# Kernel tuning notes

Hardware: AMD Instinct MI355X
Metric: run time of the kernel (lower is better)

The kernel has to match this reference:

```python
import jax, jax.numpy as jnp
import numpy as np

N = 20000      # nodes
E = 320000     # edges
IN = 128       # in_channels
HID = 64       # hidden_channels (per-head out dim, concat=False -> mean over heads)
HEADS = 4
NEG_SLOPE = 0.2


def setup_inputs() -> dict:
    key = jax.random.key(0)
    ks = jax.random.split(key, 18)
    g = lambda i, shape: jax.random.normal(ks[i], shape, dtype=jnp.float32) * 0.05
    return {
        "x": jax.random.normal(ks[0], (N, IN), dtype=jnp.float32),
        "edge_index": jax.random.randint(ks[1], (2, E), 0, N),
        # GATConv params: lin weight (no bias in PyG lin), att_src/att_dst, out bias
        "W0": g(2, (IN, HEADS * HID)),
        "W1": g(3, (HID, HEADS * HID)),
        "W2": g(4, (HID, HEADS * HID)),
        "W3": g(5, (HID, HEADS * HID)),
        "a_src": g(6, (4, HEADS, HID)),
        "a_dst": g(7, (4, HEADS, HID)),
        "gat_b": g(8, (4, HID)),
        # residual projection for layer 0 (in_channels != hidden_channels)
        "res_W": g(9, (IN, HID)),
        "res_b": g(10, (HID,)),
        # edge classifier MLP: 2*HID -> HID -> HID -> 1
        "lin_W0": g(11, (2 * HID, HID)),
        "lin_b0": g(12, (HID,)),
        "lin_W1": g(13, (HID, HID)),
        "lin_b1": g(14, (HID,)),
        "lin_W2": g(15, (HID, 1)),
        "lin_b2": g(16, (1,)),
    }


def gat_conv(x, src, dst, W, asrc, adst, b, n):
    # x: [n, F_in]; src/dst: [E_tot] (self-loops included); W: [F_in, H*C]
    h = (x @ W).reshape(n, HEADS, HID)                     # [n, H, C]
    s_src = (h * asrc).sum(-1)                             # [n, H]
    s_dst = (h * adst).sum(-1)                             # [n, H]
    e = jax.nn.leaky_relu(s_src[src] + s_dst[dst], NEG_SLOPE)  # [E_tot, H]
    # segment softmax over incoming edges of each dst node
    m = jax.ops.segment_max(e, dst, num_segments=n)        # [n, H]
    p = jnp.exp(e - m[dst])
    z = jax.ops.segment_sum(p, dst, num_segments=n)
    alpha = p / z[dst]                                     # [E_tot, H]
    out = jax.ops.segment_sum(alpha[:, :, None] * h[src], dst, num_segments=n)  # [n, H, C]
    return out.mean(axis=1) + b                            # concat=False -> mean over heads


def reference(x, edge_index, W0, W1, W2, W3, a_src, a_dst, gat_b,
              res_W, res_b, lin_W0, lin_b0, lin_W1, lin_b1, lin_W2, lin_b2):
    n = x.shape[0]
    loop = jnp.arange(n)
    src = jnp.concatenate([edge_index[0], loop])  # PyG GATConv adds self-loops
    dst = jnp.concatenate([edge_index[1], loop])
    Ws = [W0, W1, W2, W3]
    h = x
    for i in range(4):
        h_prev = h
        h = gat_conv(h, src, dst, Ws[i], a_src[i], a_dst[i], gat_b[i], n)
        if i == 0:
            h = h + h_prev @ res_W + res_b   # projected residual
        else:
            h = h + h_prev
        h = jax.nn.elu(h)
    row, col = edge_index[0], edge_index[1]
    er = jnp.concatenate([h[row], h[col]], axis=1)        # [E, 2*HID]
    er = jax.nn.relu(er @ lin_W0 + lin_b0)                # shapes differ -> no residual
    er = jax.nn.relu(er @ lin_W1 + lin_b1 + er)           # shapes match -> residual
    logits = er @ lin_W2 + lin_b2                          # [E, 1]
    return logits
```

## Files before the change

### kernel.cpp

```cpp
#include <hip/hip_runtime.h>
#include <hip/hip_bf16.h>

#define NSLOPE 0.2f
#define MAXDEG 64

typedef short bf16x8 __attribute__((ext_vector_type(8)));
typedef float f32x4 __attribute__((ext_vector_type(4)));

__device__ __forceinline__ unsigned short f2b(float f) {
    unsigned u = __float_as_uint(f);
    unsigned r = (u + 0x7FFFu + ((u >> 16) & 1u)) >> 16;
    return (unsigned short)r;
}
__device__ __forceinline__ float b2f_lo(unsigned w) {
    return __uint_as_float(w << 16);
}
__device__ __forceinline__ float b2f_hi(unsigned w) {
    return __uint_as_float(w & 0xFFFF0000u);
}
__device__ __forceinline__ float b2f_s(short s) {
    return __uint_as_float(((unsigned)(unsigned short)s) << 16);
}
__device__ __forceinline__ unsigned packb(float lo, float hi) {
    return ((unsigned)f2b(hi) << 16) | (unsigned)f2b(lo);
}

__global__ __launch_bounds__(256) void prep_all(
    const float* __restrict__ W0, const float* __restrict__ W1,
    const float* __restrict__ W2, const float* __restrict__ W3,
    const float* __restrict__ resW, const float* __restrict__ linW0,
    const float* __restrict__ linW1, const float* __restrict__ linB0,
    const float* __restrict__ a_src, const float* __restrict__ a_dst,
    const float* __restrict__ gat_b, const float* __restrict__ res_b,
    short* __restrict__ WtC0e, short* __restrict__ WtC1,
    short* __restrict__ WtC2, short* __restrict__ WtC3,
    short* __restrict__ WtUV, short* __restrict__ WbT,
    float* __restrict__ wsd0, float* __restrict__ wsdL,
    float* __restrict__ bias128, float* __restrict__ gb0res,
    int* __restrict__ deg, int n) {
    const int bx = blockIdx.x;
    const int tid = threadIdx.x;
    if (bx == 0) {
        for (int idx = blockIdx.y * 256 + tid; idx < 64 * 640; idx += 256 * 16) {
            int j = idx / 640, k = idx - j * 640;
            float v;
            if (k < 512) {
                int h = k >> 7, kk = k & 127;
                v = W0[kk * 256 + h * 64 + j];
            } else {
                v = resW[(k - 512) * 64 + j];
            }
            WtC0e[idx] = (short)f2b(v);
        }
    } else if (bx <= 3) {
        const float* src = (bx == 1) ? W1 : (bx == 2) ? W2 : W3;
        short* dst = (bx == 1) ? WtC1 : (bx == 2) ? WtC2 : WtC3;
        for (int idx = blockIdx.y * 256 + tid; idx < 64 * 256; idx += 256 * 16) {
            int j = idx >> 8, rem = idx & 255;
            int h = rem >> 6, kk = rem & 63;
            dst[idx] = (short)f2b(src[kk * 256 + h * 64 + j]);
        }
    } else if (bx == 4) {
        if (blockIdx.y) return;
        for (int idx = tid; idx < 64 * 64; idx += 256) {
            int nn = idx >> 6, k = idx & 63;
            WtUV[idx] = (short)f2b(linW0[k * 64 + nn]);
        }
    } else if (bx == 5) {
        if (blockIdx.y) return;
        for (int idx = tid; idx < 64 * 64; idx += 256) {
            int nn = idx >> 6, k = idx & 63;
            WtUV[64 * 64 + idx] = (short)f2b(linW0[(k + 64) * 64 + nn]);
        }
    } else if (bx == 6) {
        if (blockIdx.y) return;
        for (int idx = tid; idx < 64 * 64; idx += 256) {
            int nn = idx >> 6, k = idx & 63;
            WbT[idx] = (short)f2b(linW1[k * 64 + nn]);
        }
    } else if (bx == 7) {
        if (blockIdx.y) return;
        if (tid < 128)
            bias128[tid] = (tid < 64) ? linB0[tid] : 0.f;
        else if (tid < 192)
            gb0res[tid - 128] = gat_b[tid - 128] + res_b[tid - 128];
    } else if (bx <= 11) {
        if (blockIdx.y) return;
        int l = bx - 8;
        const float* W = (l == 0) ? W0 : (l == 1) ? W1 : (l == 2) ? W2 : W3;
        const int K = (l == 0) ? 128 : 64;
        float* dst = (l == 0) ? wsd0 : wsdL + (l - 1) * 64 * 8;
        for (int idx = tid; idx < K * 8; idx += 256) {
            int k = idx >> 3, j = idx & 7, h = j & 3;
            const float* av = ((j < 4) ? a_src : a_dst) + l * 256 + h * 64;
            const float* wr = W + k * 256 + h * 64;
            float s = 0.f;
#pragma unroll 8
            for (int c = 0; c < 64; ++c) s += wr[c] * av[c];
            dst[k * 8 + j] = s;
        }
    } else {
        for (int i = blockIdx.y * 256 + tid; i < n; i += 256 * 16) deg[i] = 0;
    }
}

__global__ __launch_bounds__(256) void fill_convert(
    const int* __restrict__ ei, int* __restrict__ deg,
    unsigned short* __restrict__ csrS, int E, const float* __restrict__ x,
    const float* __restrict__ wsd0, unsigned* __restrict__ xb2,
    float* __restrict__ Ssrc, float* __restrict__ Sdst, int n, int eBlocks) {
    if ((int)blockIdx.x < eBlocks) {
        int e = blockIdx.x * 256 + threadIdx.x;
        if (e >= E) return;
        int s = ei[e], d = ei[E + e];
        int pos = atomicAdd(&deg[d], 1);
        if (pos < MAXDEG) csrS[(size_t)d * MAXDEG + pos] = (unsigned short)s;
        return;
    }
    const int nb = blockIdx.x - eBlocks;
    const int wid = threadIdx.x >> 6;
    const int lane = threadIdx.x & 63;
    const int node = nb * 4 + wid;
    if (node >= n) return;
    float2 xv = *(const float2*)&x[(size_t)node * 128 + lane * 2];
    xb2[(size_t)node * 64 + lane] = packb(xv.x, xv.y);
    float pv[8];
    const float* w0 = &wsd0[(lane * 2) * 8];
    const float* w1 = &wsd0[(lane * 2 + 1) * 8];
#pragma unroll
    for (int j = 0; j < 8; ++j) pv[j] = xv.x * w0[j] + xv.y * w1[j];
#pragma unroll
    for (int off = 1; off < 64; off <<= 1) {
#pragma unroll
        for (int j = 0; j < 8; ++j) pv[j] += __shfl_xor(pv[j], off, 64);
    }
    if (lane == 0) {
        *(float4*)&Ssrc[node * 4] = make_float4(pv[0], pv[1], pv[2], pv[3]);
        *(float4*)&Sdst[node * 4] = make_float4(pv[4], pv[5], pv[6], pv[7]);
    }
}

__global__ __launch_bounds__(256) void gat_gather128(
    const unsigned short* __restrict__ csrS, const int* __restrict__ deg,
    const float* __restrict__ Ssrc, const float* __restrict__ Sdst,
    const unsigned* __restrict__ xin, unsigned* __restrict__ aggB, int n) {
    const int wid = threadIdx.x >> 6;
    const int lane = threadIdx.x & 63;
    const int node = blockIdx.x * 4 + wid;
    if (node >= n) return;
    const int dn = min(deg[node], MAXDEG);
    const int sreg = (lane < dn) ? (int)csrS[(size_t)node * MAXDEG + lane] : 0;
    const float4 sd = *(const float4*)&Sdst[node * 4];
    const float4 ss = *(const float4*)&Ssrc[node * 4];
    float c0 = ss.x + sd.x, c1 = ss.y + sd.y, c2 = ss.z + sd.z,
          c3 = ss.w + sd.w;
    c0 = c0 > 0.f ? c0 : NSLOPE * c0;
    c1 = c1 > 0.f ? c1 : NSLOPE * c1;
    c2 = c2 > 0.f ? c2 : NSLOPE * c2;
    c3 = c3 > 0.f ? c3 : NSLOPE * c3;
    float ps0 = __expf(c0), ps1 = __expf(c1), ps2 = __expf(c2),
          ps3 = __expf(c3);
    unsigned own = xin[(size_t)node * 64 + lane];
    float f0o = b2f_lo(own), f1o = b2f_hi(own);
    float u00 = ps0 * f0o, u01 = ps0 * f1o;
    float u10 = ps1 * f0o, u11 = ps1 * f1o;
    float u20 = ps2 * f0o, u21 = ps2 * f1o;
    float u30 = ps3 * f0o, u31 = ps3 * f1o;
    float z0 = ps0, z1 = ps1, z2 = ps2, z3 = ps3;
#pragma unroll 4
    for (int p = 0; p < dn; ++p) {
        int sj = __shfl(sreg, p, 64);
        float4 sv = *(const float4*)&Ssrc[sj * 4];
        unsigned fv = xin[(size_t)sj * 64 + lane];
        float e0 = sv.x + sd.x, e1 = sv.y + sd.y;
        float e2 = sv.z + sd.z, e3 = sv.w + sd.w;
        e0 = e0 > 0.f ? e0 : NSLOPE * e0;
        e1 = e1 > 0.f ? e1 : NSLOPE * e1;
        e2 = e2 > 0.f ? e2 : NSLOPE * e2;
        e3 = e3 > 0.f ? e3 : NSLOPE * e3;
        float p0 = __expf(e0), p1 = __expf(e1);
        float p2 = __expf(e2), p3 = __expf(e3);
        float f0 = b2f_lo(fv), f1 = b2f_hi(fv);
        u00 += p0 * f0; u01 += p0 * f1;
        u10 += p1 * f0; u11 += p1 * f1;
        u20 += p2 * f0; u21 += p2 * f1;
        u30 += p3 * f0; u31 += p3 * f1;
        z0 += p0; z1 += p1; z2 += p2; z3 += p3;
    }
    float i0 = 0.25f / z0, i1 = 0.25f / z1, i2 = 0.25f / z2, i3 = 0.25f / z3;
    size_t base = (size_t)node * 320;
    aggB[base + lane] = packb(u00 * i0, u01 * i0);
    aggB[base + 64 + lane] = packb(u10 * i1, u11 * i1);
    aggB[base + 128 + lane] = packb(u20 * i2, u21 * i2);
    aggB[base + 192 + lane] = packb(u30 * i3, u31 * i3);
    aggB[base + 256 + lane] = own;
}

__global__ __launch_bounds__(256) void gat_gather64(
    const unsigned short* __restrict__ csrS, const int* __restrict__ deg,
    const float* __restrict__ Ssrc, const float* __restrict__ Sdst,
    const unsigned* __restrict__ fin, unsigned* __restrict__ aggB, int n) {
    const int wid = threadIdx.x >> 6;
    const int lane = threadIdx.x & 63;
    const int half = lane >> 5;
    const int cl = lane & 31;
    const int node = blockIdx.x * 4 + wid;
    if (node >= n) return;
    const int dn = min(deg[node], MAXDEG);
    const int sreg = (lane < dn) ? (int)csrS[(size_t)node * MAXDEG + lane] : 0;
    const float4 sd = *(const float4*)&Sdst[node * 4];
    const float4 ss = *(const float4*)&Ssrc[node * 4];
    float c0 = ss.x + sd.x, c1 = ss.y + sd.y, c2 = ss.z + sd.z,
          c3 = ss.w + sd.w;
    c0 = c0 > 0.f ? c0 : NSLOPE * c0;
    c1 = c1 > 0.f ? c1 : NSLOPE * c1;
    c2 = c2 > 0.f ? c2 : NSLOPE * c2;
    c3 = c3 > 0.f ? c3 : NSLOPE * c3;
    float ps0 = __expf(c0), ps1 = __expf(c1), ps2 = __expf(c2),
          ps3 = __expf(c3);
    unsigned own = fin[(size_t)node * 32 + cl];
    float u00 = 0.f, u01 = 0.f, u10 = 0.f, u11 = 0.f;
    float u20 = 0.f, u21 = 0.f, u30 = 0.f, u31 = 0.f;
    float z0 = 0.f, z1 = 0.f, z2 = 0.f, z3 = 0.f;
#pragma unroll 4
    for (int p = half; p < dn; p += 2) {
        int sj = __shfl(sreg, p, 64);
        float4 sv = *(const float4*)&Ssrc[sj * 4];
        unsigned fv = fin[(size_t)sj * 32 + cl];
        float e0 = sv.x + sd.x, e1 = sv.y + sd.y;
        float e2 = sv.z + sd.z, e3 = sv.w + sd.w;
        e0 = e0 > 0.f ? e0 : NSLOPE * e0;
        e1 = e1 > 0.f ? e1 : NSLOPE * e1;
        e2 = e2 > 0.f ? e2 : NSLOPE * e2;
        e3 = e3 > 0.f ? e3 : NSLOPE * e3;
        float p0 = __expf(e0), p1 = __expf(e1);
        float p2 = __expf(e2), p3 = __expf(e3);
        float f0 = b2f_lo(fv), f1 = b2f_hi(fv);
        u00 += p0 * f0; u01 += p0 * f1;
        u10 += p1 * f0; u11 += p1 * f1;
        u20 += p2 * f0; u21 += p2 * f1;
        u30 += p3 * f0; u31 += p3 * f1;
        z0 += p0; z1 += p1; z2 += p2; z3 += p3;
    }
    u00 += __shfl_xor(u00, 32, 64); u01 += __shfl_xor(u01, 32, 64);
    u10 += __shfl_xor(u10, 32, 64); u11 += __shfl_xor(u11, 32, 64);
    u20 += __shfl_xor(u20, 32, 64); u21 += __shfl_xor(u21, 32, 64);
    u30 += __shfl_xor(u30, 32, 64); u31 += __shfl_xor(u31, 32, 64);
    z0 += __shfl_xor(z0, 32, 64); z1 += __shfl_xor(z1, 32, 64);
    z2 += __shfl_xor(z2, 32, 64); z3 += __shfl_xor(z3, 32, 64);
    if (half == 0) {
        float f0o = b2f_lo(own), f1o = b2f_hi(own);
        u00 += ps0 * f0o; u01 += ps0 * f1o;
        u10 += ps1 * f0o; u11 += ps1 * f1o;
        u20 += ps2 * f0o; u21 += ps2 * f1o;
        u30 += ps3 * f0o; u31 += ps3 * f1o;
        z0 += ps0; z1 += ps1; z2 += ps2; z3 += ps3;
        float i0 = 0.25f / z0, i1 = 0.25f / z1;
        float i2 = 0.25f / z2, i3 = 0.25f / z3;
        size_t base = (size_t)node * 128;
        aggB[base + cl] = packb(u00 * i0, u01 * i0);
        aggB[base + 32 + cl] = packb(u10 * i1, u11 * i1);
        aggB[base + 64 + cl] = packb(u20 * i2, u21 * i2);
        aggB[base + 96 + cl] = packb(u30 * i3, u31 * i3);
    }
}

template <int KK, bool SCORES>
__global__ __launch_bounds__(256) void gemm_layer(
    const short* __restrict__ Xb, const short* __restrict__ Wt,
    const float* __restrict__ gbias, const float* __restrict__ resid,
    const float* __restrict__ wsd, float* __restrict__ feat,
    short* __restrict__ featb, float* __restrict__ Ssrc,
    float* __restrict__ Sdst, int n) {
    __shared__ __align__(16) short Xs[64 * 136];
    __shared__ __align__(16) short Ws[64 * 40];
    const int tid = threadIdx.x;
    const int nb = blockIdx.x * 64;
    const int wid = tid >> 6;
    const int lane = tid & 63;
    const int t = lane & 15, quad = lane >> 4;
    f32x4 acc[4];
#pragma unroll
    for (int g = 0; g < 4; ++g) acc[g] = (f32x4){0.f, 0.f, 0.f, 0.f};
#pragma unroll 1
    for (int c0 = 0; c0 < KK / 128; ++c0) {
        __syncthreads();
        for (int idx = tid; idx < 1024; idx += 256) {
            int row = idx >> 4, c = idx & 15;
            uint4 v = make_uint4(0, 0, 0, 0);
            if (nb + row < n)
                v = *(const uint4*)(Xb + (size_t)(nb + row) * KK + c0 * 128 +
                                    c * 8);
            *(uint4*)(Xs + row * 136 + c * 8) = v;
        }
#pragma unroll 1
        for (int kc = 0; kc < 4; ++kc) {
            __syncthreads();
            {
                int row = tid >> 2, c = tid & 3;
                uint4 v = *(const uint4*)(Wt + (size_t)row * KK + c0 * 128 +
                                          kc * 32 + c * 8);
                *(uint4*)(Ws + row * 40 + c * 8) = v;
            }
            __syncthreads();
            bf16x8 a =
                *(const bf16x8*)(Xs + (wid * 16 + t) * 136 + kc * 32 + quad * 8);
#pragma unroll
            for (int g = 0; g < 4; ++g) {
                bf16x8 b = *(const bf16x8*)(Ws + (g * 16 + t) * 40 + quad * 8);
                acc[g] =
                    __builtin_amdgcn_mfma_f32_16x16x32_bf16(a, b, acc[g], 0, 0, 0);
            }
        }
    }
    float bv[4];
#pragma unroll
    for (int g = 0; g < 4; ++g) bv[g] = gbias[g * 16 + t];
    float wsv[4][8];
    if (SCORES) {
#pragma unroll
        for (int g = 0; g < 4; ++g) {
            float4 lo = *(const float4*)&wsd[(g * 16 + t) * 8];
            float4 hi = *(const float4*)&wsd[(g * 16 + t) * 8 + 4];
            wsv[g][0] = lo.x; wsv[g][1] = lo.y; wsv[g][2] = lo.z;
            wsv[g][3] = lo.w; wsv[g][4] = hi.x; wsv[g][5] = hi.y;
            wsv[g][6] = hi.z; wsv[g][7] = hi.w;
        }
    }
#pragma unroll
    for (int r = 0; r < 4; ++r) {
        int node = nb + wid * 16 + quad * 4 + r;
        bool ok = node < n;
        float val[4];
#pragma unroll
        for (int g = 0; g < 4; ++g) {
            float v = acc[g][r] + bv[g];
            if (resid && ok) v += resid[(size_t)node * 64 + g * 16 + t];
            v = v > 0.f ? v : expm1f(v);
            val[g] = v;
            if (ok) {
                feat[(size_t)node * 64 + g * 16 + t] = v;
                featb[(size_t)node * 64 + g * 16 + t] = (short)f2b(v);
            }
        }
        if (SCORES) {
            float pv[8];
#pragma unroll
            for (int j = 0; j < 8; ++j) {
                pv[j] = val[0] * wsv[0][j] + val[1] * wsv[1][j] +
                        val[2] * wsv[2][j] + val[3] * wsv[3][j];
            }
#pragma unroll
            for (int off = 1; off < 16; off <<= 1) {
#pragma unroll
                for (int j = 0; j < 8; ++j) pv[j] += __shfl_xor(pv[j], off, 64);
            }
            if (t == 0 && ok) {
                *(float4*)&Ssrc[node * 4] =
                    make_float4(pv[0], pv[1], pv[2], pv[3]);
                *(float4*)&Sdst[node * 4] =
                    make_float4(pv[4], pv[5], pv[6], pv[7]);
            }
        }
    }
}

__global__ __launch_bounds__(256) void gemm_layer_uv(
    const short* __restrict__ Xb, const short* __restrict__ Wt,
    const float* __restrict__ gbias, const float* __restrict__ resid,
    const short* __restrict__ WtUV, const float* __restrict__ bias128,
    short* __restrict__ OutUV, int n) {
    constexpr int KK = 256;
    __shared__ __align__(16) short Xs[64 * 136];
    __shared__ __align__(16) short Ws[128 * 40];
    const int tid = threadIdx.x;
    const int nb = blockIdx.x * 64;
    const int wid = tid >> 6;
    const int lane = tid & 63;
    const int t = lane & 15, quad = lane >> 4;
    f32x4 acc[4];
#pragma unroll
    for (int g = 0; g < 4; ++g) acc[g] = (f32x4){0.f, 0.f, 0.f, 0.f};
#pragma unroll 1
    for (int c0 = 0; c0 < KK / 128; ++c0) {
        __syncthreads();
        for (int idx = tid; idx < 1024; idx += 256) {
            int row = idx >> 4, c = idx & 15;
            uint4 v = make_uint4(0, 0, 0, 0);
            if (nb + row < n)
                v = *(const uint4*)(Xb + (size_t)(nb + row) * KK + c0 * 128 +
                                    c * 8);
            *(uint4*)(Xs + row * 136 + c * 8) = v;
        }
#pragma unroll 1
        for (int kc = 0; kc < 4; ++kc) {
            __syncthreads();
            {
                int row = tid >> 2, c = tid & 3;
                uint4 v = *(const uint4*)(Wt + (size_t)row * KK + c0 * 128 +
                                          kc * 32 + c * 8);
                *(uint4*)(Ws + row * 40 + c * 8) = v;
            }
            __syncthreads();
            bf16x8 a =
                *(const bf16x8*)(Xs + (wid * 16 + t) * 136 + kc * 32 + quad * 8);
#pragma unroll
            for (int g = 0; g < 4; ++g) {
                bf16x8 b = *(const bf16x8*)(Ws + (g * 16 + t) * 40 + quad * 8);
                acc[g] =
                    __builtin_amdgcn_mfma_f32_16x16x32_bf16(a, b, acc[g], 0, 0, 0);
            }
        }
    }
    float bv[4];
#pragma unroll
    for (int g = 0; g < 4; ++g) bv[g] = gbias[g * 16 + t];
    __syncthreads();
#pragma unroll
    for (int r = 0; r < 4; ++r) {
        int node = nb + wid * 16 + quad * 4 + r;
        bool ok = node < n;
        int lrow = wid * 16 + quad * 4 + r;
#pragma unroll
        for (int g = 0; g < 4; ++g) {
            float v = acc[g][r] + bv[g];
            if (ok) v += resid[(size_t)node * 64 + g * 16 + t];
            v = v > 0.f ? v : expm1f(v);
            Xs[lrow * 72 + g * 16 + t] = (short)f2b(v);
        }
    }
    f32x4 acc2[8];
#pragma unroll
    for (int g = 0; g < 8; ++g) acc2[g] = (f32x4){0.f, 0.f, 0.f, 0.f};
#pragma unroll 1
    for (int kc = 0; kc < 2; ++kc) {
        __syncthreads();
        for (int idx = tid; idx < 512; idx += 256) {
            int row = idx >> 2, c = idx & 3;
            uint4 v = *(const uint4*)(WtUV + (size_t)row * 64 + kc * 32 + c * 8);
            *(uint4*)(Ws + row * 40 + c * 8) = v;
        }
        __syncthreads();
        bf16x8 a = *(const bf16x8*)(Xs + (wid * 16 + t) * 72 + kc * 32 + quad * 8);
#pragma unroll
        for (int g = 0; g < 8; ++g) {
            bf16x8 b = *(const bf16x8*)(Ws + (g * 16 + t) * 40 + quad * 8);
            acc2[g] = __builtin_amdgcn_mfma_f32_16x16x32_bf16(a, b, acc2[g], 0, 0, 0);
        }
    }
    float b2[8];
#pragma unroll
    for (int g = 0; g < 8; ++g) b2[g] = bias128[g * 16 + t];
#pragma unroll
    for (int r = 0; r < 4; ++r) {
        int node = nb + wid * 16 + quad * 4 + r;
        if (node >= n) continue;
#pragma unroll
        for (int g = 0; g < 8; ++g)
            OutUV[(size_t)node * 128 + g * 16 + t] =
                (short)f2b(acc2[g][r] + b2[g]);
    }
}

__global__ __launch_bounds__(256) void edge_mlp3(
    const int* __restrict__ ei, const unsigned* __restrict__ UV,
    const short* __restrict__ WbT, const float* __restrict__ bb,
    const float* __restrict__ Wc, const float* __restrict__ bc,
    float* __restrict__ out, int E) {
    __shared__ __align__(16) short t1b[64 * 72];
    __shared__ __align__(16) short wbs[64 * 72];
    const int tid = threadIdx.x;
    const int eBase = blockIdx.x * 64;
    for (int idx = tid; idx < 512; idx += 256) {
        int row = idx >> 3, c = idx & 7;
        *(uint4*)(wbs + row * 72 + c * 8) =
            *(const uint4*)(WbT + row * 64 + c * 8);
    }
    {
        const int j = tid & 31;
        const int eg = tid >> 5;
        int rr[8], cc[8];
#pragma unroll
        for (int it = 0; it < 8; ++it) {
            int e = eBase + it * 8 + eg;
            rr[it] = (e < E) ? ei[e] : 0;
            cc[it] = (e < E) ? ei[E + e] : 0;
        }
#pragma unroll
        for (int it = 0; it < 8; ++it) {
            unsigned uu = UV[(size_t)rr[it] * 64 + j];
            unsigned vv = UV[(size_t)cc[it] * 64 + 32 + j];
            float lo = fmaxf(b2f_lo(uu) + b2f_lo(vv), 0.f);
            float hi = fmaxf(b2f_hi(uu) + b2f_hi(vv), 0.f);
            *(unsigned*)(t1b + (it * 8 + eg) * 72 + j * 2) = packb(lo, hi);
        }
    }
    __syncthreads();
    const int w = tid >> 6, lane = tid & 63;
    const int t = lane & 15, quad = lane >> 4;
    f32x4 acc[4];
#pragma unroll
    for (int g = 0; g < 4; ++g) acc[g] = (f32x4){0.f, 0.f, 0.f, 0.f};
#pragma unroll
    for (int kc = 0; kc < 2; ++kc) {
        bf16x8 a = *(const bf16x8*)(t1b + (w * 16 + t) * 72 + kc * 32 + quad * 8);
#pragma unroll
        for (int g = 0; g < 4; ++g) {
            bf16x8 b = *(const bf16x8*)(wbs + (g * 16 + t) * 72 + kc * 32 + quad * 8);
            acc[g] = __builtin_amdgcn_mfma_f32_16x16x32_bf16(a, b, acc[g], 0, 0, 0);
        }
    }
    float wcv[4], bbv[4];
#pragma unroll
    for (int g = 0; g < 4; ++g) {
        wcv[g] = Wc[g * 16 + t];
        bbv[g] = bb[g * 16 + t];
    }
    const float bcv = bc[0];
#pragma unroll
    for (int r = 0; r < 4; ++r) {
        int el = w * 16 + quad * 4 + r;
        float part = 0.f;
#pragma unroll
        for (int g = 0; g < 4; ++g) {
            float t1v = b2f_s(t1b[el * 72 + g * 16 + t]);
            float t2 = fmaxf(acc[g][r] + bbv[g] + t1v, 0.f);
            part += t2 * wcv[g];
        }
        part += __shfl_xor(part, 1, 64);
        part += __shfl_xor(part, 2, 64);
        part += __shfl_xor(part, 4, 64);
        part += __shfl_xor(part, 8, 64);
        int e = eBase + el;
        if (t == 0 && e < E) out[e] = part + bcv;
    }
}

extern "C" void kernel_launch(void* const* d_in, const int* in_sizes, int n_in,
                              void* d_out, int out_size, void* d_ws,
                              size_t ws_size, hipStream_t stream) {
    const float* x = (const float*)d_in[0];
    const int* ei = (const int*)d_in[1];
    const float* W0 = (const float*)d_in[2];
    const float* W1 = (const float*)d_in[3];
    const float* W2 = (const float*)d_in[4];
    const float* W3 = (const float*)d_in[5];
    const float* a_src = (const float*)d_in[6];
    const float* a_dst = (const float*)d_in[7];
    const float* gat_b = (const float*)d_in[8];
    const float* res_W = (const float*)d_in[9];
    const float* res_b = (const float*)d_in[10];
    const float* lin_W0 = (const float*)d_in[11];
    const float* lin_b0 = (const float*)d_in[12];
    const float* lin_W1 = (const float*)d_in[13];
    const float* lin_b1 = (const float*)d_in[14];
    const float* lin_W2 = (const float*)d_in[15];
    const float* lin_b2 = (const float*)d_in[16];
    float* out = (float*)d_out;

    const int N = in_sizes[0] / 128;
    const int E = in_sizes[1] / 2;

    char* ws = (char*)d_ws;
    unsigned* aggB = (unsigned*)ws;
    float* featA = (float*)(aggB + (size_t)N * 320);
    float* featB = featA + (size_t)N * 64;
    unsigned* xb2 = (unsigned*)(featB + (size_t)N * 64);
    unsigned* featbA = xb2 + (size_t)N * 64;
    unsigned* featbB = featbA + (size_t)N * 32;
    unsigned* UVb = featbB + (size_t)N * 32;
    float* Ssrc = (float*)(UVb + (size_t)N * 64);
    float* Sdst = Ssrc + (size_t)N * 4;
    short* WtC0e = (short*)(Sdst + (size_t)N * 4);
    short* WtC1 = WtC0e + 64 * 640;
    short* WtC2 = WtC1 + 64 * 256;
    short* WtC3 = WtC2 + 64 * 256;
    short* WtUV = WtC3 + 64 * 256;
    short* WbT = WtUV + 128 * 64;
    float* wsd0 = (float*)(WbT + 64 * 64);
    float* wsdL = wsd0 + 128 * 8;
    float* bias128 = wsdL + 3 * 64 * 8;
    float* gb0res = bias128 + 128;
    int* deg = (int*)(gb0res + 64);
    unsigned short* csrS = (unsigned short*)(deg + N);

    const int gemmBlocks = (N + 63) / 64;
    const int eBlocks = (E + 255) / 256;
    const int nodeW = (N + 3) / 4;

    prep_all<<<dim3(13, 16), 256, 0, stream>>>(
        W0, W1, W2, W3, res_W, lin_W0, lin_W1, lin_b0, a_src, a_dst, gat_b,
        res_b, WtC0e, WtC1, WtC2, WtC3, WtUV, WbT, wsd0, wsdL, bias128,
        gb0res, deg, N);
    fill_convert<<<eBlocks + nodeW, 256, 0, stream>>>(
        ei, deg, csrS, E, x, wsd0, xb2, Ssrc, Sdst, N, eBlocks);

    gat_gather128<<<nodeW, 256, 0, stream>>>(csrS, deg, Ssrc, Sdst, xb2, aggB,
                                             N);
    gemm_layer<640, true><<<gemmBlocks, 256, 0, stream>>>(
        (const short*)aggB, WtC0e, gb0res, nullptr, wsdL, featA,
        (short*)featbA, Ssrc, Sdst, N);

    gat_gather64<<<nodeW, 256, 0, stream>>>(csrS, deg, Ssrc, Sdst, featbA,
                                            aggB, N);
    gemm_layer<256, true><<<gemmBlocks, 256, 0, stream>>>(
        (const short*)aggB, WtC1, gat_b + 64, featA, wsdL + 64 * 8, featB,
        (short*)featbB, Ssrc, Sdst, N);
    gat_gather64<<<nodeW, 256, 0, stream>>>(csrS, deg, Ssrc, Sdst, featbB,
                                            aggB, N);
    gemm_layer<256, true><<<gemmBlocks, 256, 0, stream>>>(
        (const short*)aggB, WtC2, gat_b + 128, featB, wsdL + 2 * 64 * 8,
        featA, (short*)featbA, Ssrc, Sdst, N);

    gat_gather64<<<nodeW, 256, 0, stream>>>(csrS, deg, Ssrc, Sdst, featbA,
                                            aggB, N);
    gemm_layer_uv<<<gemmBlocks, 256, 0, stream>>>(
        (const short*)aggB, WtC3, gat_b + 192, featA, WtUV, bias128,
        (short*)UVb, N);

    edge_mlp3<<<(E + 63) / 64, 256, 0, stream>>>(ei, UVb, WbT, lin_b1, lin_W2,
                                                 lin_b2, out, E);
}
```

Before: 328.5 us.

## Fuse GAT gather with per-layer GEMM for layers 1-3 via shared-memory aggregation

Layers 1-3 now run one kernel each. A 1024-thread block first gathers attention-weighted neighbour features for 16 nodes into shared memory, then runs the MFMA projection, residual, ELU and next-layer score computation on them. This drops the global aggB round trip and the fp32 feature buffers. The residual is read from the bf16 input features instead of fp32, and the Ssrc/Sdst buffers are double-buffered because a layer's scores are written while other blocks still read the previous ones. The costs are small GEMM tiles that use only 4 or 8 of the 16 waves, reduced precision on the residual, and large blocks that may limit occupancy.

```diff
diff --git a/kernel.cpp b/kernel.cpp
--- a/kernel.cpp
+++ b/kernel.cpp
@@ -196,82 +196,12 @@
     aggB[base + 256 + lane] = own;
 }
 
-__global__ __launch_bounds__(256) void gat_gather64(
-    const unsigned short* __restrict__ csrS, const int* __restrict__ deg,
-    const float* __restrict__ Ssrc, const float* __restrict__ Sdst,
-    const unsigned* __restrict__ fin, unsigned* __restrict__ aggB, int n) {
-    const int wid = threadIdx.x >> 6;
-    const int lane = threadIdx.x & 63;
-    const int half = lane >> 5;
-    const int cl = lane & 31;
-    const int node = blockIdx.x * 4 + wid;
-    if (node >= n) return;
-    const int dn = min(deg[node], MAXDEG);
-    const int sreg = (lane < dn) ? (int)csrS[(size_t)node * MAXDEG + lane] : 0;
-    const float4 sd = *(const float4*)&Sdst[node * 4];
-    const float4 ss = *(const float4*)&Ssrc[node * 4];
-    float c0 = ss.x + sd.x, c1 = ss.y + sd.y, c2 = ss.z + sd.z,
-          c3 = ss.w + sd.w;
-    c0 = c0 > 0.f ? c0 : NSLOPE * c0;
-    c1 = c1 > 0.f ? c1 : NSLOPE * c1;
-    c2 = c2 > 0.f ? c2 : NSLOPE * c2;
-    c3 = c3 > 0.f ? c3 : NSLOPE * c3;
-    float ps0 = __expf(c0), ps1 = __expf(c1), ps2 = __expf(c2),
-          ps3 = __expf(c3);
-    unsigned own = fin[(size_t)node * 32 + cl];
-    float u00 = 0.f, u01 = 0.f, u10 = 0.f, u11 = 0.f;
-    float u20 = 0.f, u21 = 0.f, u30 = 0.f, u31 = 0.f;
-    float z0 = 0.f, z1 = 0.f, z2 = 0.f, z3 = 0.f;
-#pragma unroll 4
-    for (int p = half; p < dn; p += 2) {
-        int sj = __shfl(sreg, p, 64);
-        float4 sv = *(const float4*)&Ssrc[sj * 4];
-        unsigned fv = fin[(size_t)sj * 32 + cl];
-        float e0 = sv.x + sd.x, e1 = sv.y + sd.y;
-        float e2 = sv.z + sd.z, e3 = sv.w + sd.w;
-        e0 = e0 > 0.f ? e0 : NSLOPE * e0;
-        e1 = e1 > 0.f ? e1 : NSLOPE * e1;
-        e2 = e2 > 0.f ? e2 : NSLOPE * e2;
-        e3 = e3 > 0.f ? e3 : NSLOPE * e3;
-        float p0 = __expf(e0), p1 = __expf(e1);
-        float p2 = __expf(e2), p3 = __expf(e3);
-        float f0 = b2f_lo(fv), f1 = b2f_hi(fv);
-        u00 += p0 * f0; u01 += p0 * f1;
-        u10 += p1 * f0; u11 += p1 * f1;
-        u20 += p2 * f0; u21 += p2 * f1;
-        u30 += p3 * f0; u31 += p3 * f1;
-        z0 += p0; z1 += p1; z2 += p2; z3 += p3;
-    }
-    u00 += __shfl_xor(u00, 32, 64); u01 += __shfl_xor(u01, 32, 64);
-    u10 += __shfl_xor(u10, 32, 64); u11 += __shfl_xor(u11, 32, 64);
-    u20 += __shfl_xor(u20, 32, 64); u21 += __shfl_xor(u21, 32, 64);
-    u30 += __shfl_xor(u30, 32, 64); u31 += __shfl_xor(u31, 32, 64);
-    z0 += __shfl_xor(z0, 32, 64); z1 += __shfl_xor(z1, 32, 64);
-    z2 += __shfl_xor(z2, 32, 64); z3 += __shfl_xor(z3, 32, 64);
-    if (half == 0) {
-        float f0o = b2f_lo(own), f1o = b2f_hi(own);
-        u00 += ps0 * f0o; u01 += ps0 * f1o;
-        u10 += ps1 * f0o; u11 += ps1 * f1o;
-        u20 += ps2 * f0o; u21 += ps2 * f1o;
-        u30 += ps3 * f0o; u31 += ps3 * f1o;
-        z0 += ps0; z1 += ps1; z2 += ps2; z3 += ps3;
-        float i0 = 0.25f / z0, i1 = 0.25f / z1;
-        float i2 = 0.25f / z2, i3 = 0.25f / z3;
-        size_t base = (size_t)node * 128;
-        aggB[base + cl] = packb(u00 * i0, u01 * i0);
-        aggB[base + 32 + cl] = packb(u10 * i1, u11 * i1);
-        aggB[base + 64 + cl] = packb(u20 * i2, u21 * i2);
-        aggB[base + 96 + cl] = packb(u30 * i3, u31 * i3);
-    }
-}
-
-template <int KK, bool SCORES>
-__global__ __launch_bounds__(256) void gemm_layer(
+__global__ __launch_bounds__(256) void gemm_layer0(
     const short* __restrict__ Xb, const short* __restrict__ Wt,
-    const float* __restrict__ gbias, const float* __restrict__ resid,
-    const float* __restrict__ wsd, float* __restrict__ feat,
+    const float* __restrict__ gbias, const float* __restrict__ wsd,
     short* __restrict__ featb, float* __restrict__ Ssrc,
     float* __restrict__ Sdst, int n) {
+    constexpr int KK = 640;
     __shared__ __align__(16) short Xs[64 * 136];
     __shared__ __align__(16) short Ws[64 * 40];
     const int tid = threadIdx.x;
@@ -317,15 +247,13 @@
 #pragma unroll
     for (int g = 0; g < 4; ++g) bv[g] = gbias[g * 16 + t];
     float wsv[4][8];
-    if (SCORES) {
-#pragma unroll
-        for (int g = 0; g < 4; ++g) {
-            float4 lo = *(const float4*)&wsd[(g * 16 + t) * 8];
-            float4 hi = *(const float4*)&wsd[(g * 16 + t) * 8 + 4];
-            wsv[g][0] = lo.x; wsv[g][1] = lo.y; wsv[g][2] = lo.z;
-            wsv[g][3] = lo.w; wsv[g][4] = hi.x; wsv[g][5] = hi.y;
-            wsv[g][6] = hi.z; wsv[g][7] = hi.w;
-        }
+#pragma unroll
+    for (int g = 0; g < 4; ++g) {
+        float4 lo = *(const float4*)&wsd[(g * 16 + t) * 8];
+        float4 hi = *(const float4*)&wsd[(g * 16 + t) * 8 + 4];
+        wsv[g][0] = lo.x; wsv[g][1] = lo.y; wsv[g][2] = lo.z;
+        wsv[g][3] = lo.w; wsv[g][4] = hi.x; wsv[g][5] = hi.y;
+        wsv[g][6] = hi.z; wsv[g][7] = hi.w;
     }
 #pragma unroll
     for (int r = 0; r < 4; ++r) {
@@ -335,130 +263,199 @@
 #pragma unroll
         for (int g = 0; g < 4; ++g) {
             float v = acc[g][r] + bv[g];
-            if (resid && ok) v += resid[(size_t)node * 64 + g * 16 + t];
             v = v > 0.f ? v : expm1f(v);
             val[g] = v;
-            if (ok) {
-                feat[(size_t)node * 64 + g * 16 + t] = v;
-                featb[(size_t)node * 64 + g * 16 + t] = (short)f2b(v);
-            }
-        }
-        if (SCORES) {
+            if (ok) featb[(size_t)node * 64 + g * 16 + t] = (short)f2b(v);
+        }
+        float pv[8];
+#pragma unroll
+        for (int j = 0; j < 8; ++j) {
+            pv[j] = val[0] * wsv[0][j] + val[1] * wsv[1][j] +
+                    val[2] * wsv[2][j] + val[3] * wsv[3][j];
+        }
+#pragma unroll
+        for (int off = 1; off < 16; off <<= 1) {
+#pragma unroll
+            for (int j = 0; j < 8; ++j) pv[j] += __shfl_xor(pv[j], off, 64);
+        }
+        if (t == 0 && ok) {
+            *(float4*)&Ssrc[node * 4] = make_float4(pv[0], pv[1], pv[2], pv[3]);
+            *(float4*)&Sdst[node * 4] = make_float4(pv[4], pv[5], pv[6], pv[7]);
+        }
+    }
+}
+
+template <bool UV>
+__global__ __launch_bounds__(1024) void layer_fused(
+    const unsigned short* __restrict__ csrS, const int* __restrict__ deg,
+    const float* __restrict__ SsrcIn, const float* __restrict__ SdstIn,
+    const unsigned* __restrict__ fin,
+    const short* __restrict__ Wt,
+    const float* __restrict__ gbias, const float* __restrict__ wsd,
+    short* __restrict__ featbOut, float* __restrict__ SsrcOut,
+    float* __restrict__ SdstOut, const short* __restrict__ WtUV,
+    const float* __restrict__ bias128, short* __restrict__ OutUV, int n) {
+    __shared__ __align__(16) short aggL[16 * 264];
+    __shared__ __align__(16) short Ws[128 * 40];
+    __shared__ float valL[16 * 68];
+    const int tid = threadIdx.x;
+    const int w = tid >> 6;
+    const int lane = tid & 63;
+    const int half = lane >> 5;
+    const int cl = lane & 31;
+    const int nbase = blockIdx.x * 16;
+    {
+        const int node = nbase + w;
+        if (node < n) {
+            const int dn = min(deg[node], MAXDEG);
+            const int sreg =
+                (lane < dn) ? (int)csrS[(size_t)node * MAXDEG + lane] : 0;
+            const float4 sd = *(const float4*)&SdstIn[node * 4];
+            const float4 ss = *(const float4*)&SsrcIn[node * 4];
+            float c0 = ss.x + sd.x, c1 = ss.y + sd.y, c2 = ss.z + sd.z,
+                  c3 = ss.w + sd.w;
+            c0 = c0 > 0.f ? c0 : NSLOPE * c0;
+            c1 = c1 > 0.f ? c1 : NSLOPE * c1;
+            c2 = c2 > 0.f ? c2 : NSLOPE * c2;
+            c3 = c3 > 0.f ? c3 : NSLOPE * c3;
+            float ps0 = __expf(c0), ps1 = __expf(c1), ps2 = __expf(c2),
+                  ps3 = __expf(c3);
+            unsigned own = fin[(size_t)node * 32 + cl];
+            float u00 = 0.f, u01 = 0.f, u10 = 0.f, u11 = 0.f;
+            float u20 = 0.f, u21 = 0.f, u30 = 0.f, u31 = 0.f;
+            float z0 = 0.f, z1 = 0.f, z2 = 0.f, z3 = 0.f;
+#pragma unroll 4
+            for (int p = half; p < dn; p += 2) {
+                int sj = __shfl(sreg, p, 64);
+                float4 sv = *(const float4*)&SsrcIn[sj * 4];
+                unsigned fv = fin[(size_t)sj * 32 + cl];
+                float e0 = sv.x + sd.x, e1 = sv.y + sd.y;
+                float e2 = sv.z + sd.z, e3 = sv.w + sd.w;
+                e0 = e0 > 0.f ? e0 : NSLOPE * e0;
+                e1 = e1 > 0.f ? e1 : NSLOPE * e1;
+                e2 = e2 > 0.f ? e2 : NSLOPE * e2;
+                e3 = e3 > 0.f ? e3 : NSLOPE * e3;
+                float p0 = __expf(e0), p1 = __expf(e1);
+                float p2 = __expf(e2), p3 = __expf(e3);
+                float f0 = b2f_lo(fv), f1 = b2f_hi(fv);
+                u00 += p0 * f0; u01 += p0 * f1;
+                u10 += p1 * f0; u11 += p1 * f1;
+                u20 += p2 * f0; u21 += p2 * f1;
+                u30 += p3 * f0; u31 += p3 * f1;
+                z0 += p0; z1 += p1; z2 += p2; z3 += p3;
+            }
+            u00 += __shfl_xor(u00, 32, 64); u01 += __shfl_xor(u01, 32, 64);
+            u10 += __shfl_xor(u10, 32, 64); u11 += __shfl_xor(u11, 32, 64);
+            u20 += __shfl_xor(u20, 32, 64); u21 += __shfl_xor(u21, 32, 64);
+            u30 += __shfl_xor(u30, 32, 64); u31 += __shfl_xor(u31, 32, 64);
+            z0 += __shfl_xor(z0, 32, 64); z1 += __shfl_xor(z1, 32, 64);
+            z2 += __shfl_xor(z2, 32, 64); z3 += __shfl_xor(z3, 32, 64);
+            if (half == 0) {
+                float f0o = b2f_lo(own), f1o = b2f_hi(own);
+                u00 += ps0 * f0o; u01 += ps0 * f1o;
+                u10 += ps1 * f0o; u11 += ps1 * f1o;
+                u20 += ps2 * f0o; u21 += ps2 * f1o;
+                u30 += ps3 * f0o; u31 += ps3 * f1o;
+                z0 += ps0; z1 += ps1; z2 += ps2; z3 += ps3;
+                float i0 = 0.25f / z0, i1 = 0.25f / z1;
+                float i2 = 0.25f / z2, i3 = 0.25f / z3;
+                unsigned* row = (unsigned*)(aggL + w * 264);
+                row[cl] = packb(u00 * i0, u01 * i0);
+                row[32 + cl] = packb(u10 * i1, u11 * i1);
+                row[64 + cl] = packb(u20 * i2, u21 * i2);
+                row[96 + cl] = packb(u30 * i3, u31 * i3);
+            }
+        }
+    }
+    __syncthreads();
+    const int t = lane & 15, quad = lane >> 4;
+    f32x4 acc = (f32x4){0.f, 0.f, 0.f, 0.f};
+#pragma unroll 1
+    for (int kc = 0; kc < 8; ++kc) {
+        __syncthreads();
+        if (tid < 256) {
+            int row = tid >> 2, c = tid & 3;
+            *(uint4*)(Ws + row * 40 + c * 8) =
+                *(const uint4*)(Wt + (size_t)row * 256 + kc * 32 + c * 8);
+        }
+        __syncthreads();
+        if (w < 4) {
+            bf16x8 a = *(const bf16x8*)(aggL + t * 264 + kc * 32 + quad * 8);
+            bf16x8 b = *(const bf16x8*)(Ws + (w * 16 + t) * 40 + quad * 8);
+            acc = __builtin_amdgcn_mfma_f32_16x16x32_bf16(a, b, acc, 0, 0, 0);
+        }
+    }
+    if (w < 4) {
+        float bv = gbias[w * 16 + t];
+#pragma unroll
+        for (int r = 0; r < 4; ++r) {
+            int row = quad * 4 + r;
+            int node = nbase + row;
+            float v = acc[r] + bv;
+            if (node < n) {
+                unsigned rp = fin[(size_t)node * 32 + (w * 8 + (t >> 1))];
+                v += (t & 1) ? b2f_hi(rp) : b2f_lo(rp);
+                v = v > 0.f ? v : expm1f(v);
+                valL[row * 68 + w * 16 + t] = v;
+                if (!UV)
+                    featbOut[(size_t)node * 64 + w * 16 + t] = (short)f2b(v);
+            } else {
+                valL[row * 68 + w * 16 + t] = 0.f;
+            }
+        }
+    }
+    __syncthreads();
+    if (!UV) {
+        int node = nbase + w;
+        if (node < n) {
+            float v = valL[w * 68 + lane];
             float pv[8];
-#pragma unroll
-            for (int j = 0; j < 8; ++j) {
-                pv[j] = val[0] * wsv[0][j] + val[1] * wsv[1][j] +
-                        val[2] * wsv[2][j] + val[3] * wsv[3][j];
-            }
-#pragma unroll
-            for (int off = 1; off < 16; off <<= 1) {
+            const float* wsr = &wsd[lane * 8];
+#pragma unroll
+            for (int j = 0; j < 8; ++j) pv[j] = v * wsr[j];
+#pragma unroll
+            for (int off = 1; off < 64; off <<= 1) {
 #pragma unroll
                 for (int j = 0; j < 8; ++j) pv[j] += __shfl_xor(pv[j], off, 64);
             }
-            if (t == 0 && ok) {
-                *(float4*)&Ssrc[node * 4] =
+            if (lane == 0) {
+                *(float4*)&SsrcOut[node * 4] =
                     make_float4(pv[0], pv[1], pv[2], pv[3]);
-                *(float4*)&Sdst[node * 4] =
+                *(float4*)&SdstOut[node * 4] =
                     make_float4(pv[4], pv[5], pv[6], pv[7]);
             }
         }
-    }
-}
-
-__global__ __launch_bounds__(256) void gemm_layer_uv(
-    const short* __restrict__ Xb, const short* __restrict__ Wt,
-    const float* __restrict__ gbias, const float* __restrict__ resid,
-    const short* __restrict__ WtUV, const float* __restrict__ bias128,
-    short* __restrict__ OutUV, int n) {
-    constexpr int KK = 256;
-    __shared__ __align__(16) short Xs[64 * 136];
-    __shared__ __align__(16) short Ws[128 * 40];
-    const int tid = threadIdx.x;
-    const int nb = blockIdx.x * 64;
-    const int wid = tid >> 6;
-    const int lane = tid & 63;
-    const int t = lane & 15, quad = lane >> 4;
-    f32x4 acc[4];
-#pragma unroll
-    for (int g = 0; g < 4; ++g) acc[g] = (f32x4){0.f, 0.f, 0.f, 0.f};
+    } else {
+        {
+            int row = tid >> 6, col = tid & 63;
+            aggL[row * 72 + col] = (short)f2b(valL[row * 68 + col]);
+        }
+        f32x4 acc2 = (f32x4){0.f, 0.f, 0.f, 0.f};
 #pragma unroll 1
-    for (int c0 = 0; c0 < KK / 128; ++c0) {
-        __syncthreads();
-        for (int idx = tid; idx < 1024; idx += 256) {
-            int row = idx >> 4, c = idx & 15;
-            uint4 v = make_uint4(0, 0, 0, 0);
-            if (nb + row < n)
-                v = *(const uint4*)(Xb + (size_t)(nb + row) * KK + c0 * 128 +
-                                    c * 8);
-            *(uint4*)(Xs + row * 136 + c * 8) = v;
-        }
-#pragma unroll 1
-        for (int kc = 0; kc < 4; ++kc) {
+        for (int kc = 0; kc < 2; ++kc) {
             __syncthreads();
-            {
+            if (tid < 512) {
                 int row = tid >> 2, c = tid & 3;
-                uint4 v = *(const uint4*)(Wt + (size_t)row * KK + c0 * 128 +
-                                          kc * 32 + c * 8);
-                *(uint4*)(Ws + row * 40 + c * 8) = v;
+                *(uint4*)(Ws + row * 40 + c * 8) =
+                    *(const uint4*)(WtUV + (size_t)row * 64 + kc * 32 + c * 8);
             }
             __syncthreads();
-            bf16x8 a =
-                *(const bf16x8*)(Xs + (wid * 16 + t) * 136 + kc * 32 + quad * 8);
-#pragma unroll
-            for (int g = 0; g < 4; ++g) {
-                bf16x8 b = *(const bf16x8*)(Ws + (g * 16 + t) * 40 + quad * 8);
-                acc[g] =
-                    __builtin_amdgcn_mfma_f32_16x16x32_bf16(a, b, acc[g], 0, 0, 0);
-            }
-        }
-    }
-    float bv[4];
-#pragma unroll
-    for (int g = 0; g < 4; ++g) bv[g] = gbias[g * 16 + t];
-    __syncthreads();
-#pragma unroll
-    for (int r = 0; r < 4; ++r) {
-        int node = nb + wid * 16 + quad * 4 + r;
-        bool ok = node < n;
-        int lrow = wid * 16 + quad * 4 + r;
-#pragma unroll
-        for (int g = 0; g < 4; ++g) {
-            float v = acc[g][r] + bv[g];
-            if (ok) v += resid[(size_t)node * 64 + g * 16 + t];
-            v = v > 0.f ? v : expm1f(v);
-            Xs[lrow * 72 + g * 16 + t] = (short)f2b(v);
-        }
-    }
-    f32x4 acc2[8];
-#pragma unroll
-    for (int g = 0; g < 8; ++g) acc2[g] = (f32x4){0.f, 0.f, 0.f, 0.f};
-#pragma unroll 1
-    for (int kc = 0; kc < 2; ++kc) {
-        __syncthreads();
-        for (int idx = tid; idx < 512; idx += 256) {
-            int row = idx >> 2, c = idx & 3;
-            uint4 v = *(const uint4*)(WtUV + (size_t)row * 64 + kc * 32 + c * 8);
-            *(uint4*)(Ws + row * 40 + c * 8) = v;
-        }
-        __syncthreads();
-        bf16x8 a = *(const bf16x8*)(Xs + (wid * 16 + t) * 72 + kc * 32 + quad * 8);
-#pragma unroll
-        for (int g = 0; g < 8; ++g) {
-            bf16x8 b = *(const bf16x8*)(Ws + (g * 16 + t) * 40 + quad * 8);
-            acc2[g] = __builtin_amdgcn_mfma_f32_16x16x32_bf16(a, b, acc2[g], 0, 0, 0);
-        }
-    }
-    float b2[8];
-#pragma unroll
-    for (int g = 0; g < 8; ++g) b2[g] = bias128[g * 16 + t];
-#pragma unroll
-    for (int r = 0; r < 4; ++r) {
-        int node = nb + wid * 16 + quad * 4 + r;
-        if (node >= n) continue;
-#pragma unroll
-        for (int g = 0; g < 8; ++g)
-            OutUV[(size_t)node * 128 + g * 16 + t] =
-                (short)f2b(acc2[g][r] + b2[g]);
+            if (w < 8) {
+                bf16x8 a = *(const bf16x8*)(aggL + t * 72 + kc * 32 + quad * 8);
+                bf16x8 b = *(const bf16x8*)(Ws + (w * 16 + t) * 40 + quad * 8);
+                acc2 = __builtin_amdgcn_mfma_f32_16x16x32_bf16(a, b, acc2, 0, 0, 0);
+            }
+        }
+        if (w < 8) {
+            float b2v = bias128[w * 16 + t];
+#pragma unroll
+            for (int r = 0; r < 4; ++r) {
+                int node = nbase + quad * 4 + r;
+                if (node < n)
+                    OutUV[(size_t)node * 128 + w * 16 + t] =
+                        (short)f2b(acc2[r] + b2v);
+            }
+        }
     }
 }
 
@@ -563,15 +560,15 @@
 
     char* ws = (char*)d_ws;
     unsigned* aggB = (unsigned*)ws;
-    float* featA = (float*)(aggB + (size_t)N * 320);
-    float* featB = featA + (size_t)N * 64;
-    unsigned* xb2 = (unsigned*)(featB + (size_t)N * 64);
+    unsigned* xb2 = aggB + (size_t)N * 320;
     unsigned* featbA = xb2 + (size_t)N * 64;
     unsigned* featbB = featbA + (size_t)N * 32;
     unsigned* UVb = featbB + (size_t)N * 32;
-    float* Ssrc = (float*)(UVb + (size_t)N * 64);
-    float* Sdst = Ssrc + (size_t)N * 4;
-    short* WtC0e = (short*)(Sdst + (size_t)N * 4);
+    float* SsrcA = (float*)(UVb + (size_t)N * 64);
+    float* SdstA = SsrcA + (size_t)N * 4;
+    float* SsrcB = SdstA + (size_t)N * 4;
+    float* SdstB = SsrcB + (size_t)N * 4;
+    short* WtC0e = (short*)(SdstB + (size_t)N * 4);
     short* WtC1 = WtC0e + 64 * 640;
     short* WtC2 = WtC1 + 64 * 256;
     short* WtC3 = WtC2 + 64 * 256;
@@ -587,36 +584,30 @@
     const int gemmBlocks = (N + 63) / 64;
     const int eBlocks = (E + 255) / 256;
     const int nodeW = (N + 3) / 4;
+    const int fusedBlocks = (N + 15) / 16;
 
     prep_all<<<dim3(13, 16), 256, 0, stream>>>(
         W0, W1, W2, W3, res_W, lin_W0, lin_W1, lin_b0, a_src, a_dst, gat_b,
         res_b, WtC0e, WtC1, WtC2, WtC3, WtUV, WbT, wsd0, wsdL, bias128,
         gb0res, deg, N);
     fill_convert<<<eBlocks + nodeW, 256, 0, stream>>>(
-        ei, deg, csrS, E, x, wsd0, xb2, Ssrc, Sdst, N, eBlocks);
-
-    gat_gather128<<<nodeW, 256, 0, stream>>>(csrS, deg, Ssrc, Sdst, xb2, aggB,
-                                             N);
-    gemm_layer<640, true><<<gemmBlocks, 256, 0, stream>>>(
-        (const short*)aggB, WtC0e, gb0res, nullptr, wsdL, featA,
-        (short*)featbA, Ssrc, Sdst, N);
-
-    gat_gather64<<<nodeW, 256, 0, stream>>>(csrS, deg, Ssrc, Sdst, featbA,
-                                            aggB, N);
-    gemm_layer<256, true><<<gemmBlocks, 256, 0, stream>>>(
-        (const short*)aggB, WtC1, gat_b + 64, featA, wsdL + 64 * 8, featB,
-        (short*)featbB, Ssrc, Sdst, N);
-    gat_gather64<<<nodeW, 256, 0, stream>>>(csrS, deg, Ssrc, Sdst, featbB,
-                                            aggB, N);
-    gemm_layer<256, true><<<gemmBlocks, 256, 0, stream>>>(
-        (const short*)aggB, WtC2, gat_b + 128, featB, wsdL + 2 * 64 * 8,
-        featA, (short*)featbA, Ssrc, Sdst, N);
-
-    gat_gather64<<<nodeW, 256, 0, stream>>>(csrS, deg, Ssrc, Sdst, featbA,
-                                            aggB, N);
-    gemm_layer_uv<<<gemmBlocks, 256, 0, stream>>>(
-        (const short*)aggB, WtC3, gat_b + 192, featA, WtUV, bias128,
-        (short*)UVb, N);
+        ei, deg, csrS, E, x, wsd0, xb2, SsrcA, SdstA, N, eBlocks);
+
+    gat_gather128<<<nodeW, 256, 0, stream>>>(csrS, deg, SsrcA, SdstA, xb2,
+                                             aggB, N);
+    gemm_layer0<<<gemmBlocks, 256, 0, stream>>>((const short*)aggB, WtC0e,
+                                                gb0res, wsdL, (short*)featbA,
+                                                SsrcB, SdstB, N);
+
+    layer_fused<false><<<fusedBlocks, 1024, 0, stream>>>(
+        csrS, deg, SsrcB, SdstB, featbA, WtC1, gat_b + 64, wsdL + 64 * 8,
+        (short*)featbB, SsrcA, SdstA, nullptr, nullptr, nullptr, N);
+    layer_fused<false><<<fusedBlocks, 1024, 0, stream>>>(
+        csrS, deg, SsrcA, SdstA, featbB, WtC2, gat_b + 128, wsdL + 2 * 64 * 8,
+        (short*)featbA, SsrcB, SdstB, nullptr, nullptr, nullptr, N);
+    layer_fused<true><<<fusedBlocks, 1024, 0, stream>>>(
+        csrS, deg, SsrcB, SdstB, featbA, WtC3, gat_b + 192, nullptr, nullptr,
+        nullptr, nullptr, WtUV, bias128, (short*)UVb, N);
 
     edge_mlp3<<<(E + 63) / 64, 256, 0, stream>>>(ei, UVb, WbT, lin_b1, lin_W2,
                                                  lin_b2, out, E);
```

New measurement: 331.5 us. Within noise of the previous version (+0.9%).
